# Kernel tuning notes

Hardware: AMD Instinct MI355X
Metric: run time of the kernel (lower is better)

Reference implementation:

```python
import jax, jax.numpy as jnp
import numpy as np


def _dconv(x, W, b, d):
    # dilated 3x3 conv, padding=d so spatial size is preserved (NCHW / OIHW)
    y = jax.lax.conv_general_dilated(
        x, W, window_strides=(1, 1), padding=((d, d), (d, d)),
        rhs_dilation=(d, d), dimension_numbers=('NCHW', 'OIHW', 'NCHW'))
    return y + b[None, :, None, None]


def setup_inputs() -> dict:
    key = jax.random.key(0)
    ks = jax.random.split(key, 12)
    B, C, H, W = 2, 512, 64, 64
    s = 0.02  # keep pre-softmax energies in a sane range
    inp = {
        'x':  jax.random.normal(ks[0], (B, C, H, W), jnp.float32),
        'W1': jax.random.normal(ks[1], (128, 512, 3, 3), jnp.float32) * s,
        'b1': jnp.zeros((128,), jnp.float32),
        'W2': jax.random.normal(ks[2], (128, 512, 3, 3), jnp.float32) * s,
        'b2': jnp.zeros((128,), jnp.float32),
        'W3': jax.random.normal(ks[3], (128, 512, 3, 3), jnp.float32) * s,
        'b3': jnp.zeros((128,), jnp.float32),
        'W4': jax.random.normal(ks[4], (128, 512, 3, 3), jnp.float32) * s,
        'b4': jnp.zeros((128,), jnp.float32),
        'Wd':  jax.random.normal(ks[5], (512, 128), jnp.float32) * s,   # dense, 1x1 no bias
        'Wcc': jax.random.normal(ks[6], (256, 512), jnp.float32) * s,   # CCIFL conv 512->256
        'bcc': jnp.zeros((256,), jnp.float32),
        'Wd2': jax.random.normal(ks[7], (512, 256), jnp.float32) * s,   # dense2, 1x1 no bias
    }
    return inp


def reference(x, W1, b1, W2, b2, W3, b3, W4, b4, Wd, Wcc, bcc, Wd2):
    B, C, H, W = x.shape
    N = H * W
    # four dilated-conv feature maps, flattened to [B, 128, N]
    a1 = jax.nn.relu(_dconv(x, W1, b1, 2)).reshape(B, 128, N)
    a2 = jax.nn.relu(_dconv(x, W2, b2, 3)).reshape(B, 128, N)
    a3 = jax.nn.relu(_dconv(x, W3, b3, 5)).reshape(B, 128, N)
    a4 = jax.nn.relu(_dconv(x, W4, b4, 7)).reshape(B, 128, N)

    # spatial attention 1: softmax(a1^T a2), applied as a4 @ att
    att12 = jax.nn.softmax(jnp.einsum('bcn,bcm->bnm', a1, a2), axis=-1)
    o1 = jnp.einsum('bcn,bnm->bcm', a4, att12).reshape(B, 128, H, W)
    o1 = jnp.einsum('oc,bchw->bohw', Wd, o1)  # dense 128->512

    # spatial attention 2: softmax(a3^T a4), applied as a2 @ att
    att34 = jax.nn.softmax(jnp.einsum('bcn,bcm->bnm', a3, a4), axis=-1)
    o2 = jnp.einsum('bcn,bnm->bcm', a2, att34).reshape(B, 128, H, W)
    o2 = jnp.einsum('oc,bchw->bohw', Wd, o2)

    def ccifl(y):
        # GAP -> 1x1 conv (512->256) -> scalar qk attention (softmax over a 1x1 -> 1)
        g = jnp.mean(y, axis=(2, 3))                        # [B, 512]
        z = jnp.einsum('oc,bc->bo', Wcc, g) + bcc           # [B, 256]
        e = jnp.einsum('bc,bc->b', z, z)[:, None, None]     # [B, 1, 1]
        att = jax.nn.softmax(e, axis=-1)                    # == 1
        return z * att[:, 0, :]                             # [B, 256]

    c1 = jnp.einsum('oc,bc->bo', Wd2, ccifl(o1))            # [B, 512]
    c2 = jnp.einsum('oc,bc->bo', Wd2, ccifl(o2))
    # broadcast [B,512,1,1] channel attention over spatial dims + residual
    return c1[:, :, None, None] + c2[:, :, None, None] + x
```

## Files before the change

kernel.cpp:

```cpp
#include <hip/hip_runtime.h>
#include <hip/hip_bf16.h>

typedef short short8 __attribute__((ext_vector_type(8)));
typedef float f32x4 __attribute__((ext_vector_type(4)));
typedef unsigned short u16;

#define XT_OFF   0
#define XT_BYTES (2*78*78*512*2)
#define WR2_OFF  (XT_OFF + XT_BYTES)
#define WR2_BYTES (2*9*16*8*64*16)
#define AFTER_W  (WR2_OFF + WR2_BYTES)
#define P_OFF    AFTER_W
#define P_BYTES  (4*4*128*4096*2)
#define GA_OFF_P (P_OFF + P_BYTES)
#define CA_OFF   AFTER_W
#define CA_BYTES (4*4096*128*4)
#define GA_OFF_A (CA_OFF + CA_BYTES)
#define GA_BYTES 2048
#define GV_REL   GA_BYTES
#define ZV_REL   (GV_REL + 4*512*4)
#define TAIL_END (ZV_REL + 4*256*4)
#define WS_NEED_P ((size_t)GA_OFF_P + TAIL_END)
#define WS_NEED_A ((size_t)GA_OFF_A + TAIL_END)

static __device__ __forceinline__ void async_cp16(u16* lds, const u16* g) {
  __builtin_amdgcn_global_load_lds(
      (const __attribute__((address_space(1))) void*)g,
      (__attribute__((address_space(3))) void*)lds, 16, 0, 0);
}

__global__ void zero_u4(uint4* __restrict__ p, int n) {
  int i = blockIdx.x * blockDim.x + threadIdx.x;
  int st = gridDim.x * blockDim.x;
  uint4 z = {0u, 0u, 0u, 0u};
  for (; i < n; i += st) p[i] = z;
}

__global__ void prep_all(const float* __restrict__ x, u16* __restrict__ xT,
                         const float* __restrict__ W2, const float* __restrict__ W4,
                         u16* __restrict__ Wr2) {
  int bid = blockIdx.x;
  int t = threadIdx.x;
  if (bid < 1024) {
    __shared__ float tile[64][65];
    int bh = bid >> 3, cc = bid & 7;
    int b = bh >> 6, h = bh & 63;
    int w = t & 63, cq4 = t >> 6;
    int pi = t >> 2, q = t & 3;
#pragma unroll
    for (int i = 0; i < 16; ++i) {
      int ci = cq4 + i * 4;
      tile[ci][w] = x[((b * 512 + cc * 64 + ci) * 4096) + h * 64 + w];
    }
    __syncthreads();
    union { u16 u[16]; uint4 v[2]; } pk;
#pragma unroll
    for (int k = 0; k < 16; ++k) {
      __hip_bfloat16 hb = __float2bfloat16(tile[q * 16 + k][pi]);
      pk.u[k] = *(u16*)&hb;
    }
    u16* dst = xT + ((size_t)(b * 78 + h + 7) * 78 + (pi + 7)) * 512 + cc * 64 + q * 16;
    *(uint4*)dst = pk.v[0];
    *(uint4*)(dst + 8) = pk.v[1];
  } else if (bid < 1312) {
    int hb = bid - 1024;
    size_t off; int cnt;
    if (hb < 256) {
      int b = hb >> 7, rem = hb & 127, h = rem >> 1, side = rem & 1;
      off = ((size_t)(b * 78 + 7 + h) * 78 + (side ? 71 : 0)) * 512;
      cnt = 7 * 512;
    } else {
      int k = hb - 256;
      int b = k >> 4, topbot = (k >> 3) & 1, ch = k & 7;
      off = ((size_t)b * 78 + (topbot ? 71 : 0)) * 78 * 512 + (size_t)ch * 34944;
      cnt = 34944;
    }
    uint4* p = (uint4*)(xT + off);
    int n = cnt >> 3;
    uint4 z = {0u, 0u, 0u, 0u};
    for (int i = t; i < n; i += blockDim.x) p[i] = z;
  } else {
    int idx = bid - 1312;
    int conv = idx >> 7, o = idx & 127;
    const float* W = conv ? W4 : W2;
    __shared__ float sw[4608];
    const float* src = W + (size_t)o * 4608;
    for (int k = 0; k < 18; ++k) sw[t + k * 256] = src[t + k * 256];
    __syncthreads();
    if (t < 144) {
      int tap = t >> 4, kc = t & 15;
      int wn = o >> 6, ni = (o >> 4) & 3;
      size_t base = (size_t)conv * 589824 + (size_t)(tap * 16 + kc) * 4096
                    + (wn * 4 + ni) * 512;
#pragma unroll
      for (int cg = 0; cg < 4; ++cg) {
        union { u16 h[8]; uint4 v; } pk;
#pragma unroll
        for (int e = 0; e < 8; ++e) {
          __hip_bfloat16 hb = __float2bfloat16(sw[(kc * 32 + cg * 8 + e) * 9 + tap]);
          pk.h[e] = *(u16*)&hb;
        }
        int lane = cg * 16 + (o & 15);
        *(uint4*)(Wr2 + base + lane * 8) = pk.v;
      }
    }
  }
}

template<int MODE>
__global__ __launch_bounds__(256, 2) void conv_mfma(
    const u16* __restrict__ xT, const u16* __restrict__ Wr2,
    u16* __restrict__ Pp, float* __restrict__ convacc) {
  __shared__ __align__(16) u16 Ab[2][8192];
  int bid = blockIdx.x;
  int xcd = bid & 7, cq = (bid >> 3) & 3, conv = (bid >> 5) & 1;
  int pthi = (bid >> 6) & 3, b = bid >> 8;
  int pt = pthi * 8 + xcd;
  int u = conv * 2 + b;
  int d = conv ? 7 : 3;
  int h0 = pt * 2;
  const u16* xb = xT + (size_t)b * (78 * 78 * 512);
  int t = threadIdx.x, l = t & 63, wv = t >> 6;

  int slog = (l & 7) ^ (l >> 3);
  int wq = wv * 8 + (l >> 3);
  const u16* gA[4];
#pragma unroll
  for (int m = 0; m < 4; ++m) {
    int hh = m >> 1, mh = m & 1;
    gA[m] = xb + ((size_t)(h0 + hh - d + 7) * 78 + (mh * 32 + wq - d + 7)) * 512
            + cq * 128 + slog * 8;
  }
  const char* bB = (const char*)Wr2 + (size_t)conv * 1179648
                   + cq * 32768 + wv * 2048 + l * 16;

  int rbase = (l & 15) * 64;
  int rs0 = (((l >> 4)) ^ (l & 7)) * 8;
  int rs1 = ((4 + (l >> 4)) ^ (l & 7)) * 8;

  f32x4 acc[8][2];
#pragma unroll
  for (int i = 0; i < 8; ++i)
#pragma unroll
    for (int jj = 0; jj < 2; ++jj) acc[i][jj] = (f32x4){0.f, 0.f, 0.f, 0.f};

  short8 bf0[2][2], bf1[2][2];

  auto issueA = [&](int buf) {
#pragma unroll
    for (int m = 0; m < 4; ++m)
      async_cp16(&Ab[buf][m * 2048 + wv * 512], gA[m]);
    __builtin_amdgcn_sched_barrier(0);
  };
  auto loadB = [&](short8 bf[2][2]) {
#pragma unroll
    for (int c01 = 0; c01 < 2; ++c01)
#pragma unroll
      for (int ni = 0; ni < 2; ++ni)
        bf[c01][ni] = *(const short8*)(bB + c01 * 8192 + ni * 1024);
  };
  auto cbar = [&]() {
    __builtin_amdgcn_sched_barrier(0);
    asm volatile("s_waitcnt vmcnt(4)" ::: "memory");
    __builtin_amdgcn_s_barrier();
    __builtin_amdgcn_sched_barrier(0);
  };
  auto advance = [&](int s) {
    int dA, dB;
    if (!(s & 1)) { dA = 64; dB = 16384; }
    else {
      dB = 114688;
      int tap = (s + 1) >> 1;
      dA = (tap % 3) ? (512 * d - 64) : (38912 * d - 64);
    }
#pragma unroll
    for (int m = 0; m < 4; ++m) gA[m] += dA;
    bB += dB;
  };
  auto compute = [&](int buf, short8 bf[2][2]) {
    const u16* A = Ab[buf];
#pragma unroll
    for (int mi = 0; mi < 8; ++mi) {
      short8 a0 = *(const short8*)&A[rbase + mi * 1024 + rs0];
      short8 a1 = *(const short8*)&A[rbase + mi * 1024 + rs1];
      acc[mi][0] = __builtin_amdgcn_mfma_f32_16x16x32_bf16(a0, bf[0][0], acc[mi][0], 0, 0, 0);
      acc[mi][1] = __builtin_amdgcn_mfma_f32_16x16x32_bf16(a0, bf[0][1], acc[mi][1], 0, 0, 0);
      acc[mi][0] = __builtin_amdgcn_mfma_f32_16x16x32_bf16(a1, bf[1][0], acc[mi][0], 0, 0, 0);
      acc[mi][1] = __builtin_amdgcn_mfma_f32_16x16x32_bf16(a1, bf[1][1], acc[mi][1], 0, 0, 0);
    }
  };

  issueA(0); loadB(bf0); advance(0);
  cbar();
  for (int it = 0; it < 9; ++it) {
    int s = it * 2;
    issueA(1); loadB(bf1); advance(s + 1);
    compute(0, bf0);
    cbar();
    if (it < 8) { issueA(0); loadB(bf0); advance(s + 2); }
    compute(1, bf1);
    cbar();
  }

  if (MODE == 0) {
    u16* L = (u16*)Ab;
#pragma unroll
    for (int mi = 0; mi < 8; ++mi)
#pragma unroll
      for (int ni = 0; ni < 2; ++ni) {
        int oc = wv * 32 + ni * 16 + (l & 15);
        int chunk = mi * 4 + (l >> 4);
        int chs = chunk ^ ((l & 15) << 1);
        __hip_bfloat16 h0 = __float2bfloat16(acc[mi][ni][0]);
        __hip_bfloat16 h1 = __float2bfloat16(acc[mi][ni][1]);
        __hip_bfloat16 h2 = __float2bfloat16(acc[mi][ni][2]);
        __hip_bfloat16 h3 = __float2bfloat16(acc[mi][ni][3]);
        uint2 v;
        v.x = (unsigned)*(u16*)&h0 | ((unsigned)*(u16*)&h1 << 16);
        v.y = (unsigned)*(u16*)&h2 | ((unsigned)*(u16*)&h3 << 16);
        *(uint2*)&L[oc * 128 + chs * 4] = v;
      }
    __syncthreads();
    size_t gbase = (size_t)(cq * 4 + u) * 128 * 4096 + pt * 128;
#pragma unroll
    for (int k = 0; k < 8; ++k) {
      int C = t + k * 256;
      int r = C >> 4, ci = C & 15;
      int ch0 = (2 * ci) ^ ((r & 15) << 1);
      uint4 vv = *(const uint4*)&L[r * 128 + ch0 * 4];
      *(uint4*)(Pp + gbase + (size_t)r * 4096 + ci * 8) = vv;
    }
  } else {
    float* ca = convacc + (size_t)u * 4096 * 128;
#pragma unroll
    for (int mi = 0; mi < 8; ++mi)
#pragma unroll
      for (int ni = 0; ni < 2; ++ni)
#pragma unroll
        for (int jj = 0; jj < 4; ++jj) {
          int pos = pt * 128 + mi * 16 + (l >> 4) * 4 + jj;
          int oc = wv * 32 + ni * 16 + (l & 15);
          atomicAdd(&ca[pos * 128 + oc], acc[mi][ni][jj]);
        }
  }
}

__global__ void reduce_gap_p(const u16* __restrict__ P,
                             const float* __restrict__ b2, const float* __restrict__ b4,
                             float* __restrict__ gapacc) {
  int u = blockIdx.x >> 7, oc = blockIdx.x & 127;
  const float* bias = (u >> 1) ? b4 : b2;
  int t = threadIdx.x;
  float bi = bias[oc];
  const u16* p0 = P + ((size_t)u * 128 + oc) * 4096 + t * 16;
  float v[16];
#pragma unroll
  for (int k = 0; k < 16; ++k) v[k] = bi;
#pragma unroll
  for (int cq = 0; cq < 4; ++cq) {
    const u16* pp = p0 + (size_t)cq * 2097152;
    uint4 a = *(const uint4*)pp;
    uint4 bq = *(const uint4*)(pp + 8);
    unsigned w[8] = {a.x, a.y, a.z, a.w, bq.x, bq.y, bq.z, bq.w};
#pragma unroll
    for (int k = 0; k < 8; ++k) {
      v[2 * k]     += __builtin_bit_cast(float, (w[k] & 0xffffu) << 16);
      v[2 * k + 1] += __builtin_bit_cast(float, w[k] & 0xffff0000u);
    }
  }
  float s = 0.f;
#pragma unroll
  for (int k = 0; k < 16; ++k) s += v[k] > 0.f ? v[k] : 0.f;
#pragma unroll
  for (int m = 1; m < 64; m <<= 1) s += __shfl_xor(s, m);
  __shared__ float red[4];
  if ((t & 63) == 0) red[t >> 6] = s;
  __syncthreads();
  if (t == 0) gapacc[u * 128 + oc] = red[0] + red[1] + red[2] + red[3];
}

__global__ void reduce_gap_a(const float* __restrict__ convacc,
                             const float* __restrict__ b2, const float* __restrict__ b4,
                             float* __restrict__ gapacc) {
  int unit = blockIdx.x >> 5, chunk = blockIdx.x & 31;
  int conv = unit >> 1;
  const float* bias = conv ? b4 : b2;
  int t = threadIdx.x, oc = t & 127, half = t >> 7;
  const float* ca = convacc + (size_t)unit * 4096 * 128;
  float bi = bias[oc];
  float s = 0.f;
  for (int i = 0; i < 64; ++i) {
    int pos = chunk * 128 + half * 64 + i;
    float v = ca[pos * 128 + oc] + bi;
    s += v > 0.f ? v : 0.f;
  }
  __shared__ float red[2][128];
  red[half][oc] = s;
  __syncthreads();
  if (t < 128) atomicAdd(&gapacc[unit * 128 + t], red[0][t] + red[1][t]);
}

__global__ void dense1(const float* __restrict__ gapacc, const float* __restrict__ Wd,
                       float* __restrict__ gv) {
  int o = blockIdx.x, t = threadIdx.x;
  float w = Wd[o * 128 + t];
  float p0 = w * gapacc[2 * 128 + t];
  float p1 = w * gapacc[0 * 128 + t];
  float p2 = w * gapacc[3 * 128 + t];
  float p3 = w * gapacc[1 * 128 + t];
#pragma unroll
  for (int m = 1; m < 64; m <<= 1) {
    p0 += __shfl_xor(p0, m); p1 += __shfl_xor(p1, m);
    p2 += __shfl_xor(p2, m); p3 += __shfl_xor(p3, m);
  }
  __shared__ float red[2][4];
  if ((t & 63) == 0) {
    red[t >> 6][0] = p0; red[t >> 6][1] = p1;
    red[t >> 6][2] = p2; red[t >> 6][3] = p3;
  }
  __syncthreads();
  if (t < 4) {
    const float inv = 1.f / 4096.f;
    gv[t * 512 + o] = (red[0][t] + red[1][t]) * inv;
  }
}

__global__ void dense2(const float* __restrict__ gv, const float* __restrict__ Wcc,
                       const float* __restrict__ bcc, float* __restrict__ zv) {
  int o = blockIdx.x, t = threadIdx.x;
  float w0 = Wcc[o * 512 + t], w1 = Wcc[o * 512 + 256 + t];
  float p[4];
#pragma unroll
  for (int c = 0; c < 4; ++c)
    p[c] = w0 * gv[c * 512 + t] + w1 * gv[c * 512 + 256 + t];
#pragma unroll
  for (int m = 1; m < 64; m <<= 1)
#pragma unroll
    for (int c = 0; c < 4; ++c) p[c] += __shfl_xor(p[c], m);
  __shared__ float red[4][4];
  if ((t & 63) == 0)
#pragma unroll
    for (int c = 0; c < 4; ++c) red[t >> 6][c] = p[c];
  __syncthreads();
  if (t < 4) {
    float s = bcc[o];
#pragma unroll
    for (int wv = 0; wv < 4; ++wv) s += red[wv][t];
    zv[t * 256 + o] = s;
  }
}

__global__ void final_add(const float* __restrict__ x, const float* __restrict__ zv,
                          const float* __restrict__ Wd2, float* __restrict__ out) {
  int t = threadIdx.x, bid = blockIdx.x;
  int ch = (bid >> 2) & 511;
  float w = Wd2[ch * 256 + t];
  float p0 = w * (zv[t] + zv[256 + t]);
  float p1 = w * (zv[512 + t] + zv[768 + t]);
#pragma unroll
  for (int m = 1; m < 64; m <<= 1) {
    p0 += __shfl_xor(p0, m);
    p1 += __shfl_xor(p1, m);
  }
  __shared__ float red[4][2];
  __shared__ float cv[2];
  if ((t & 63) == 0) { red[t >> 6][0] = p0; red[t >> 6][1] = p1; }
  __syncthreads();
  if (t < 2) cv[t] = red[0][t] + red[1][t] + red[2][t] + red[3][t];
  __syncthreads();
  const float4* x4 = (const float4*)x;
  float4* o4 = (float4*)out;
  int i = bid * 256 + t;
  float c0 = cv[0], c1 = cv[1];
  float4 v = x4[i];
  v.x += c0; v.y += c0; v.z += c0; v.w += c0;
  o4[i] = v;
  i += 524288;
  float4 v2 = x4[i];
  v2.x += c1; v2.y += c1; v2.z += c1; v2.w += c1;
  o4[i] = v2;
}

extern "C" void kernel_launch(void* const* d_in, const int* in_sizes, int n_in,
                              void* d_out, int out_size, void* d_ws, size_t ws_size,
                              hipStream_t stream) {
  const float* x   = (const float*)d_in[0];
  const float* W2  = (const float*)d_in[3];
  const float* b2  = (const float*)d_in[4];
  const float* W4  = (const float*)d_in[7];
  const float* b4  = (const float*)d_in[8];
  const float* Wd  = (const float*)d_in[9];
  const float* Wcc = (const float*)d_in[10];
  const float* bcc = (const float*)d_in[11];
  const float* Wd2 = (const float*)d_in[12];
  float* out = (float*)d_out;

  char* ws = (char*)d_ws;
  u16* xT  = (u16*)(ws + XT_OFF);
  u16* Wr2 = (u16*)(ws + WR2_OFF);

  const bool partial = ws_size >= WS_NEED_P;
  size_t ga_off = partial ? GA_OFF_P : GA_OFF_A;
  float* gapacc = (float*)(ws + ga_off);
  float* gv     = (float*)(ws + ga_off + GV_REL);
  float* zv     = (float*)(ws + ga_off + ZV_REL);

  prep_all<<<1568, 256, 0, stream>>>(x, xT, W2, W4, Wr2);

  if (partial) {
    u16* Pp = (u16*)(ws + P_OFF);
    conv_mfma<0><<<512, 256, 0, stream>>>(xT, Wr2, Pp, nullptr);
    reduce_gap_p<<<512, 256, 0, stream>>>(Pp, b2, b4, gapacc);
  } else {
    float* convacc = (float*)(ws + CA_OFF);
    zero_u4<<<512, 256, 0, stream>>>((uint4*)convacc, (CA_BYTES + GA_BYTES) / 16);
    conv_mfma<1><<<512, 256, 0, stream>>>(xT, Wr2, nullptr, convacc);
    reduce_gap_a<<<128, 256, 0, stream>>>(convacc, b2, b4, gapacc);
  }

  dense1<<<512, 128, 0, stream>>>(gapacc, Wd, gv);
  dense2<<<256, 256, 0, stream>>>(gv, Wcc, bcc, zv);
  final_add<<<2048, 256, 0, stream>>>(x, zv, Wd2, out);
}
```

Baseline: 53.73 us.

## Double conv block tile to 256 positions with 8 waves sharing weight loads

The conv MFMA kernel now runs 512-thread blocks covering four image rows (256 positions) instead of two. Waves are arranged as a 2x4 grid over M and N, so each weight fragment loaded from global memory feeds twice as many output positions, and the A tile in shared memory doubles to 64 KB. This halves the grid to 256 blocks, aiming to cut redundant B-operand traffic at the cost of more LDS per block, lower occupancy and fewer blocks to fill the GPU.

```diff
diff --git a/kernel.cpp b/kernel.cpp
--- a/kernel.cpp
+++ b/kernel.cpp
@@ -108,33 +108,32 @@
 }
 
 template<int MODE>
-__global__ __launch_bounds__(256, 2) void conv_mfma(
+__global__ __launch_bounds__(512, 2) void conv_mfma(
     const u16* __restrict__ xT, const u16* __restrict__ Wr2,
     u16* __restrict__ Pp, float* __restrict__ convacc) {
-  __shared__ __align__(16) u16 Ab[2][8192];
+  __shared__ __align__(16) u16 Ab[2][16384];
   int bid = blockIdx.x;
   int xcd = bid & 7, cq = (bid >> 3) & 3, conv = (bid >> 5) & 1;
-  int pthi = (bid >> 6) & 3, b = bid >> 8;
+  int b = (bid >> 6) & 1, pthi = bid >> 7;
   int pt = pthi * 8 + xcd;
   int u = conv * 2 + b;
   int d = conv ? 7 : 3;
-  int h0 = pt * 2;
+  int h0 = pt * 4;
   const u16* xb = xT + (size_t)b * (78 * 78 * 512);
   int t = threadIdx.x, l = t & 63, wv = t >> 6;
-
-  int slog = (l & 7) ^ (l >> 3);
-  int wq = wv * 8 + (l >> 3);
+  int wm = wv >> 2, wn = wv & 3;
+
+  int srow = t >> 3, slot = t & 7;
+  int slog = slot ^ (srow & 7);
   const u16* gA[4];
 #pragma unroll
-  for (int m = 0; m < 4; ++m) {
-    int hh = m >> 1, mh = m & 1;
-    gA[m] = xb + ((size_t)(h0 + hh - d + 7) * 78 + (mh * 32 + wq - d + 7)) * 512
+  for (int m = 0; m < 4; ++m)
+    gA[m] = xb + ((size_t)(h0 + m - d + 7) * 78 + (srow - d + 7)) * 512
             + cq * 128 + slog * 8;
-  }
   const char* bB = (const char*)Wr2 + (size_t)conv * 1179648
-                   + cq * 32768 + wv * 2048 + l * 16;
-
-  int rbase = (l & 15) * 64;
+                   + cq * 32768 + wn * 2048 + l * 16;
+
+  int rbase = (wm * 128 + (l & 15)) * 64;
   int rs0 = (((l >> 4)) ^ (l & 7)) * 8;
   int rs1 = ((4 + (l >> 4)) ^ (l & 7)) * 8;
 
@@ -149,7 +148,7 @@
   auto issueA = [&](int buf) {
 #pragma unroll
     for (int m = 0; m < 4; ++m)
-      async_cp16(&Ab[buf][m * 2048 + wv * 512], gA[m]);
+      async_cp16(&Ab[buf][m * 4096 + wv * 512], gA[m]);
     __builtin_amdgcn_sched_barrier(0);
   };
   auto loadB = [&](short8 bf[2][2]) {
@@ -208,26 +207,26 @@
     for (int mi = 0; mi < 8; ++mi)
 #pragma unroll
       for (int ni = 0; ni < 2; ++ni) {
-        int oc = wv * 32 + ni * 16 + (l & 15);
-        int chunk = mi * 4 + (l >> 4);
+        int oc = wn * 32 + ni * 16 + (l & 15);
+        int chunk = wm * 32 + mi * 4 + (l >> 4);
         int chs = chunk ^ ((l & 15) << 1);
-        __hip_bfloat16 h0 = __float2bfloat16(acc[mi][ni][0]);
-        __hip_bfloat16 h1 = __float2bfloat16(acc[mi][ni][1]);
-        __hip_bfloat16 h2 = __float2bfloat16(acc[mi][ni][2]);
-        __hip_bfloat16 h3 = __float2bfloat16(acc[mi][ni][3]);
+        __hip_bfloat16 h0v = __float2bfloat16(acc[mi][ni][0]);
+        __hip_bfloat16 h1v = __float2bfloat16(acc[mi][ni][1]);
+        __hip_bfloat16 h2v = __float2bfloat16(acc[mi][ni][2]);
+        __hip_bfloat16 h3v = __float2bfloat16(acc[mi][ni][3]);
         uint2 v;
-        v.x = (unsigned)*(u16*)&h0 | ((unsigned)*(u16*)&h1 << 16);
-        v.y = (unsigned)*(u16*)&h2 | ((unsigned)*(u16*)&h3 << 16);
-        *(uint2*)&L[oc * 128 + chs * 4] = v;
+        v.x = (unsigned)*(u16*)&h0v | ((unsigned)*(u16*)&h1v << 16);
+        v.y = (unsigned)*(u16*)&h2v | ((unsigned)*(u16*)&h3v << 16);
+        *(uint2*)&L[oc * 256 + chs * 4] = v;
       }
     __syncthreads();
-    size_t gbase = (size_t)(cq * 4 + u) * 128 * 4096 + pt * 128;
+    size_t gbase = (size_t)(cq * 4 + u) * 128 * 4096 + pt * 256;
 #pragma unroll
     for (int k = 0; k < 8; ++k) {
-      int C = t + k * 256;
-      int r = C >> 4, ci = C & 15;
+      int C = t + k * 512;
+      int r = C >> 5, ci = C & 31;
       int ch0 = (2 * ci) ^ ((r & 15) << 1);
-      uint4 vv = *(const uint4*)&L[r * 128 + ch0 * 4];
+      uint4 vv = *(const uint4*)&L[r * 256 + ch0 * 4];
       *(uint4*)(Pp + gbase + (size_t)r * 4096 + ci * 8) = vv;
     }
   } else {
@@ -238,8 +237,8 @@
       for (int ni = 0; ni < 2; ++ni)
 #pragma unroll
         for (int jj = 0; jj < 4; ++jj) {
-          int pos = pt * 128 + mi * 16 + (l >> 4) * 4 + jj;
-          int oc = wv * 32 + ni * 16 + (l & 15);
+          int pos = pt * 256 + wm * 128 + mi * 16 + (l >> 4) * 4 + jj;
+          int oc = wn * 32 + ni * 16 + (l & 15);
           atomicAdd(&ca[pos * 128 + oc], acc[mi][ni][jj]);
         }
   }
@@ -409,12 +408,12 @@
 
   if (partial) {
     u16* Pp = (u16*)(ws + P_OFF);
-    conv_mfma<0><<<512, 256, 0, stream>>>(xT, Wr2, Pp, nullptr);
+    conv_mfma<0><<<256, 512, 0, stream>>>(xT, Wr2, Pp, nullptr);
     reduce_gap_p<<<512, 256, 0, stream>>>(Pp, b2, b4, gapacc);
   } else {
     float* convacc = (float*)(ws + CA_OFF);
     zero_u4<<<512, 256, 0, stream>>>((uint4*)convacc, (CA_BYTES + GA_BYTES) / 16);
-    conv_mfma<1><<<512, 256, 0, stream>>>(xT, Wr2, nullptr, convacc);
+    conv_mfma<1><<<256, 512, 0, stream>>>(xT, Wr2, nullptr, convacc);
     reduce_gap_a<<<128, 256, 0, stream>>>(convacc, b2, b4, gapacc);
   }
 
```

Measured after the change: 55.87 us. 1.04x slower.
